# Optimization experiments

Hardware: AMD Instinct MI355X
Metric: run time of the kernel (lower is better)

## Reference

```python
import jax, jax.numpy as jnp
import numpy as np

B, S, D, H = 4, 1024, 1024, 16
DH = D // H
THETA = 10000.0
LAMBDA_INIT = 0.2  # layer 0: 0.8 - 0.6*exp(-0.3*0)
EPS = 1e-5


def setup_inputs() -> dict:
    key = jax.random.key(0)
    ks = jax.random.split(key, 10)
    s = 0.02
    return {
        "x_norm": jax.random.normal(ks[0], (B, S, D), jnp.float32),
        "affinity_a": jax.random.uniform(ks[1], (B, S - 1), jnp.float32, 0.5, 1.0),
        "Wq": jax.random.normal(ks[2], (2 * D, D), jnp.float32) * s,
        "bq": jnp.zeros((2 * D,), jnp.float32),
        "Wk": jax.random.normal(ks[3], (2 * D, D), jnp.float32) * s,
        "bk": jnp.zeros((2 * D,), jnp.float32),
        "Wv": jax.random.normal(ks[4], (D, D), jnp.float32) * s,
        "bv": jnp.zeros((D,), jnp.float32),
        "Wo": jax.random.normal(ks[5], (D, D), jnp.float32) * s,
        "bo": jnp.zeros((D,), jnp.float32),
        "gn_w": jnp.ones((D,), jnp.float32),
        "gn_b": jnp.zeros((D,), jnp.float32),
        "lam": jnp.float32(0.5),
    }


def _rope(x):
    # x: [B, H, S, DH]; rotate-half RoPE as in the torch module
    pos = jnp.arange(S, dtype=jnp.float32)
    freqs = 1.0 / (THETA ** (jnp.arange(0, DH, 2, dtype=jnp.float32) / DH))
    ang = pos[:, None] * freqs[None, :]          # [S, DH/2]
    cos, sin = jnp.cos(ang), jnp.sin(ang)
    x1, x2 = x[..., : DH // 2], x[..., DH // 2 :]
    return jnp.concatenate([x1 * cos - x2 * sin, x1 * sin + x2 * cos], axis=-1)


def _hier_mask(a):
    # C[b,i,j] = prod_{k=min(i,j)}^{max(i,j)-1} a[b,k]; diag = 1.
    # Vectorized via prefix log-sum instead of the O(S^2) python loop.
    logL = jnp.concatenate([jnp.zeros((a.shape[0], 1), a.dtype), jnp.cumsum(jnp.log(a), axis=1)], axis=1)  # [B, S]
    diff = logL[:, None, :] - logL[:, :, None]   # [B, i, j] = L_j - L_i
    upper = jnp.arange(S)[None, :] >= jnp.arange(S)[:, None]
    return jnp.exp(jnp.where(upper, diff, -diff))  # [B, S, S]


def _split_heads(t):
    return t.reshape(B, S, H, DH).transpose(0, 2, 1, 3)  # [B,H,S,DH]


def reference(x_norm, affinity_a, Wq, bq, Wk, bk, Wv, bv, Wo, bo, gn_w, gn_b, lam):
    qp = x_norm @ Wq.T + bq                      # [B,S,2D]
    kp = x_norm @ Wk.T + bk
    vp = x_norm @ Wv.T + bv                      # [B,S,D]
    q1, q2 = _split_heads(qp[..., :D]), _split_heads(qp[..., D:])
    k1, k2 = _split_heads(kp[..., :D]), _split_heads(kp[..., D:])
    v = _split_heads(vp)

    q1, k1, q2, k2 = _rope(q1), _rope(k1), _rope(q2), _rope(k2)

    scale = 1.0 / jnp.sqrt(jnp.float32(DH))
    a1 = jax.nn.softmax(jnp.einsum("bhid,bhjd->bhij", q1, k1) * scale, axis=-1)
    a2 = jax.nn.softmax(jnp.einsum("bhid,bhjd->bhij", q2, k2) * scale, axis=-1)

    C = _hier_mask(affinity_a)[:, None]          # [B,1,S,S]
    combined = C * (a1 - lam * a2)               # [B,H,S,S]
    ctx = jnp.einsum("bhij,bhjd->bhid", combined, v)   # [B,H,S,DH]
    ctx = ctx.transpose(0, 2, 1, 3).reshape(B, S, D)

    # GroupNorm(n_heads, d_model) applied over [B, D, S]: per (batch, group)
    # stats over the group's DH channels AND all S positions.
    xr = ctx.reshape(B, S, H, DH)
    mean = xr.mean(axis=(1, 3), keepdims=True)
    var = ((xr - mean) ** 2).mean(axis=(1, 3), keepdims=True)
    normed = (xr - mean) / jnp.sqrt(var + EPS)
    normed = normed * gn_w.reshape(1, 1, H, DH) + gn_b.reshape(1, 1, H, DH)
    normed = normed.reshape(B, S, D)

    scaled = normed * (1.0 - LAMBDA_INIT)
    return scaled @ Wo.T + bo                    # [B,S,D]
```

## Files before the change

### kernel.cpp

```cpp
#include <hip/hip_runtime.h>
#include <math.h>

typedef float  f32x4  __attribute__((ext_vector_type(4)));
typedef short  bf16x8 __attribute__((ext_vector_type(8)));
typedef unsigned short u16;

__device__ __forceinline__ u16 f2b(float f) {
  union { float f; unsigned u; } v; v.f = f;
  unsigned r = v.u + 0x7FFFu + ((v.u >> 16) & 1u);
  return (u16)(r >> 16);
}
__device__ __forceinline__ float b2f(u16 h) {
  union { unsigned u; float f; } v; v.u = ((unsigned)h) << 16;
  return v.f;
}

__device__ __forceinline__ void gl_lds16(const u16* g, u16* l) {
  __builtin_amdgcn_global_load_lds(
      (const __attribute__((address_space(1))) unsigned*)g,
      (__attribute__((address_space(3))) unsigned*)l, 16, 0, 0);
}

__global__ __launch_bounds__(256) void convert_kernel(
    const float* __restrict__ x,  const float* __restrict__ Wq,
    const float* __restrict__ Wk, const float* __restrict__ Wv,
    const float* __restrict__ Wo, const float* __restrict__ bq,
    const float* __restrict__ bk, const float* __restrict__ bv,
    const float* __restrict__ aff,
    u16* __restrict__ xb, u16* __restrict__ Wcat, u16* __restrict__ Wob,
    float* __restrict__ bcat, float* __restrict__ logL,
    float* __restrict__ ctab, float* __restrict__ stab)
{
  int bid = blockIdx.x;
  if (bid < 10245) {
    long i = ((long)bid * 256 + threadIdx.x) * 4;
    if (i < 10485760L) {
      const float* src; u16* dst; long o;
      if (i < 4194304L)      { src = x;  dst = xb;             o = i; }
      else if (i < 6291456L) { src = Wq; dst = Wcat;           o = i - 4194304L; }
      else if (i < 8388608L) { src = Wk; dst = Wcat + 2097152; o = i - 6291456L; }
      else if (i < 9437184L) { src = Wv; dst = Wcat + 4194304; o = i - 8388608L; }
      else                   { src = Wo; dst = Wob;            o = i - 9437184L; }
      float4 v = *(const float4*)(src + o);
      union { u16 h[4]; uint2 u2; } p;
      p.h[0] = f2b(v.x); p.h[1] = f2b(v.y); p.h[2] = f2b(v.z); p.h[3] = f2b(v.w);
      *(uint2*)(dst + o) = p.u2;
    } else if (i < 10490880L) {
      long j = i - 10485760L;
      const float* src; long o;
      if (j < 2048)      { src = bq; o = j; }
      else if (j < 4096) { src = bk; o = j - 2048; }
      else               { src = bv; o = j - 4096; }
      *(float4*)(bcat + j) = *(const float4*)(src + o);
    }
  } else if (bid < 10249) {
    __shared__ float sh[256];
    int b = bid - 10245, t = threadIdx.x;
    float c0, c1, c2, c3;
    {
      int i0 = 4 * t;
      float l0 = (i0 == 0) ? 0.f : log2f(aff[b * 1023 + i0 - 1]);
      float l1 = log2f(aff[b * 1023 + i0]);
      float l2 = log2f(aff[b * 1023 + i0 + 1]);
      float l3 = log2f(aff[b * 1023 + i0 + 2]);
      c0 = l0; c1 = c0 + l1; c2 = c1 + l2; c3 = c2 + l3;
    }
    sh[t] = c3;
    __syncthreads();
    for (int off = 1; off < 256; off <<= 1) {
      float add = (t >= off) ? sh[t - off] : 0.f;
      __syncthreads();
      sh[t] += add;
      __syncthreads();
    }
    float base = sh[t] - c3;
    float* Lp = logL + b * 1024 + 4 * t;
    Lp[0] = base + c0; Lp[1] = base + c1; Lp[2] = base + c2; Lp[3] = base + c3;
  } else {
    int idx = (bid - 10249) * 256 + threadIdx.x;
    int s = idx >> 5, i = idx & 31;
    float freq = expf(-(float)i * (9.210340371976184f / 32.f));
    float ang = (float)s * freq;
    ctab[idx] = cosf(ang);
    stab[idx] = sinf(ang);
  }
}

template<int EPI>
__global__ __launch_bounds__(256) void gemm_nt(
    const u16* __restrict__ A, const u16* __restrict__ Bw,
    const float* __restrict__ bias, float* __restrict__ outF,
    u16* __restrict__ q1t, u16* __restrict__ q2t,
    u16* __restrict__ k1t, u16* __restrict__ k2t, u16* __restrict__ vtT,
    const float* __restrict__ ctab, const float* __restrict__ stab,
    int N)
{
  const int K = 1024;
  __shared__ u16 As[128 * 64];
  __shared__ u16 Bs[128 * 64];
  int tid  = threadIdx.x;
  int lane = tid & 63, wave = tid >> 6;
  int wm = wave >> 1, wn = wave & 1;
  int m0 = blockIdx.y * 128, n0 = blockIdx.x * 128;
  int fr = lane & 15, hi = lane >> 4;

  int ac_r[4], ac_sb[4], cb_[4];
#pragma unroll
  for (int p = 0; p < 4; ++p) {
    int c = p * 256 + wave * 64 + lane;
    ac_r[p]  = c >> 3;
    ac_sb[p] = (c & 7) ^ (ac_r[p] & 7);
    cb_[p]   = (p * 256 + wave * 64) * 8;
  }

  f32x4 acc[4][4];
#pragma unroll
  for (int i = 0; i < 4; ++i)
#pragma unroll
    for (int j = 0; j < 4; ++j) acc[i][j] = 0.0f;

  for (int kk0 = 0; kk0 < K; kk0 += 64) {
    __syncthreads();
#pragma unroll
    for (int p = 0; p < 4; ++p) {
      gl_lds16(A  + (size_t)(m0 + ac_r[p]) * K + kk0 + ac_sb[p] * 8, &As[cb_[p]]);
      gl_lds16(Bw + (size_t)(n0 + ac_r[p]) * K + kk0 + ac_sb[p] * 8, &Bs[cb_[p]]);
    }
    __syncthreads();
#pragma unroll
    for (int ks = 0; ks < 2; ++ks) {
      bf16x8 af[4], bfv[4];
#pragma unroll
      for (int f = 0; f < 4; ++f) {
        int ra = wm * 64 + f * 16 + fr;
        int rb = wn * 64 + f * 16 + fr;
        int cba = (ks * 4 + hi) ^ (ra & 7);
        int cbb = (ks * 4 + hi) ^ (rb & 7);
        af[f]  = *(const bf16x8*)&As[ra * 64 + (cba << 3)];
        bfv[f] = *(const bf16x8*)&Bs[rb * 64 + (cbb << 3)];
      }
#pragma unroll
      for (int i = 0; i < 4; ++i)
#pragma unroll
        for (int j = 0; j < 4; ++j)
          acc[i][j] = __builtin_amdgcn_mfma_f32_16x16x32_bf16(af[i], bfv[j], acc[i][j], 0, 0, 0);
    }
  }

  int rg = lane >> 4;
  if (EPI == 0) {
    if (n0 < 4096) {
      u16* dst; int base;
      if (n0 < 1024)      { dst = q1t; base = 0; }
      else if (n0 < 2048) { dst = q2t; base = 1024; }
      else if (n0 < 3072) { dst = k1t; base = 2048; }
      else                { dst = k2t; base = 3072; }
      float qs = (n0 < 2048) ? 0.18033688011112042f : 1.0f;
#pragma unroll
      for (int i = 0; i < 4; ++i) {
#pragma unroll
        for (int e = 0; e < 4; ++e) {
          int m = m0 + wm * 64 + i * 16 + rg * 4 + e;
          int b = m >> 10, s = m & 1023;
#pragma unroll
          for (int j = 0; j < 2; ++j) {
            int n_lo = n0 + wn * 64 + j * 16 + fr;
            int feat = n_lo - base;
            int h = feat >> 6, dh = feat & 63;
            float a1 = acc[i][j][e]     + bias[n_lo];
            float a2 = acc[i][j + 2][e] + bias[n_lo + 32];
            float cs = ctab[s * 32 + dh], sn = stab[s * 32 + dh];
            float r0 = (a1 * cs - a2 * sn) * qs;
            float r1 = (a1 * sn + a2 * cs) * qs;
            unsigned pk;
            asm("v_cvt_pk_bf16_f32 %0, %1, %2" : "=v"(pk) : "v"(r0), "v"(r1));
            size_t rowb = ((size_t)(b * 16 + h) * 1024 + s) * 64;
            *(unsigned*)&dst[rowb + 2 * dh] = pk;
          }
        }
      }
    } else {
#pragma unroll
      for (int i = 0; i < 4; ++i) {
        int mbase = m0 + wm * 64 + i * 16 + rg * 4;
        int b = mbase >> 10, s0 = mbase & 1023;
#pragma unroll
        for (int j = 0; j < 4; ++j) {
          int n = n0 + wn * 64 + j * 16 + fr;
          int feat = n - 4096;
          int h = feat >> 6, dh = feat & 63;
          float bv = bias[n];
          union { u16 hh[4]; uint2 u2; } p;
#pragma unroll
          for (int e = 0; e < 4; ++e) p.hh[e] = f2b(acc[i][j][e] + bv);
          *(uint2*)&vtT[((size_t)(b * 16 + h) * 64 + dh) * 1024 + s0] = p.u2;
        }
      }
    }
  } else {
#pragma unroll
    for (int i = 0; i < 4; ++i)
#pragma unroll
      for (int j = 0; j < 4; ++j)
#pragma unroll
        for (int e = 0; e < 4; ++e) {
          int m = m0 + wm * 64 + i * 16 + rg * 4 + e;
          int n = n0 + wn * 64 + j * 16 + fr;
          outF[(size_t)m * N + n] = acc[i][j][e] + bias[n];
        }
  }
}

__global__ __launch_bounds__(256) void attn_fused(
    const u16* __restrict__ q1t, const u16* __restrict__ q2t,
    const u16* __restrict__ k1t, const u16* __restrict__ k2t,
    const u16* __restrict__ vtT,
    const float* __restrict__ logL, const float* __restrict__ lamp,
    u16* __restrict__ ctxb, float2* __restrict__ partials)
{
  __shared__ u16 K1s[64][72];
  __shared__ u16 K2s[64][72];
  __shared__ u16 Vts[64][72];
  __shared__ float lred1[2][2][32];
  __shared__ float lred2[2][2][32];
  __shared__ float pred[4][2];

  int tid  = threadIdx.x;
  int lane = tid & 63, wave = tid >> 6;
  int wm = wave >> 1, wn = wave & 1;
  int id = blockIdx.x;
  int bh = (id & 7) * 8 + (id >> 7);
  int q0 = ((id >> 3) & 15) * 64;
  int b = bh >> 4;
  int fr = lane & 15, hi = lane >> 4;

  bf16x8 qf1[2][2], qf2[2][2];
#pragma unroll
  for (int i = 0; i < 2; ++i)
#pragma unroll
    for (int ks = 0; ks < 2; ++ks) {
      size_t off = ((size_t)bh * 1024 + q0 + wm * 32 + i * 16 + fr) * 64 + ks * 32 + hi * 8;
      qf1[i][ks] = *(const bf16x8*)(q1t + off);
      qf2[i][ks] = *(const bf16x8*)(q2t + off);
    }
  float Lq[2][4];
#pragma unroll
  for (int i = 0; i < 2; ++i)
#pragma unroll
    for (int r = 0; r < 4; ++r)
      Lq[i][r] = logL[b * 1024 + q0 + wm * 32 + i * 16 + hi * 4 + r];

  float Lq_top = logL[b * 1024 + q0];
  float Lq_bot = logL[b * 1024 + q0 + 63];

  float lacc1[2][4], lacc2[2][4];
  f32x4 U1[2][2], U2[2][2];
#pragma unroll
  for (int i = 0; i < 2; ++i)
#pragma unroll
    for (int r = 0; r < 4; ++r) { lacc1[i][r] = 0.f; lacc2[i][r] = 0.f; }
#pragma unroll
  for (int i = 0; i < 2; ++i)
#pragma unroll
    for (int j = 0; j < 2; ++j) { U1[i][j] = 0.f; U2[i][j] = 0.f; }

  int sr = tid >> 2, sc0 = (tid & 3) * 16;
  int swz = (sr >> 3) & 7;
  int blk0 = ((sc0 >> 3) ^ swz) << 3;
  int blk1 = (((sc0 >> 3) + 1) ^ swz) << 3;

  unsigned a1base = (unsigned)(size_t)&K1s[wm * 32 + hi * 4][wn * 32 + fr];
  unsigned a2base = (unsigned)(size_t)&K2s[wm * 32 + hi * 4][wn * 32 + fr];

  for (int kt = 0; kt < 16; ++kt) {
    int ktop = kt * 64;
    float maxc;
    if (ktop > q0 + 63)      maxc = logL[b * 1024 + ktop] - Lq_bot;
    else if (ktop + 63 < q0) maxc = Lq_top - logL[b * 1024 + ktop + 63];
    else                     maxc = 0.f;
    bool far = (maxc < -24.f);

    __syncthreads();
    size_t gb = ((size_t)bh * 1024 + kt * 64 + sr) * 64 + sc0;
    bf16x8 a0 = *(const bf16x8*)(k1t + gb), a1 = *(const bf16x8*)(k1t + gb + 8);
    bf16x8 b0 = *(const bf16x8*)(k2t + gb), b1 = *(const bf16x8*)(k2t + gb + 8);
    *(bf16x8*)&K1s[sr][sc0] = a0;  *(bf16x8*)&K1s[sr][sc0 + 8] = a1;
    *(bf16x8*)&K2s[sr][sc0] = b0;  *(bf16x8*)&K2s[sr][sc0 + 8] = b1;
    if (!far) {
      size_t gv = (size_t)bh * 65536 + (size_t)sr * 1024 + kt * 64 + sc0;
      bf16x8 v0 = *(const bf16x8*)(vtT + gv), v1 = *(const bf16x8*)(vtT + gv + 8);
      *(bf16x8*)&Vts[sr][blk0] = v0;  *(bf16x8*)&Vts[sr][blk1] = v1;
    }
    __syncthreads();

    f32x4 S1[2][2], S2[2][2];
#pragma unroll
    for (int i = 0; i < 2; ++i)
#pragma unroll
      for (int j = 0; j < 2; ++j) { S1[i][j] = 0.f; S2[i][j] = 0.f; }
    __builtin_amdgcn_s_setprio(1);
#pragma unroll
    for (int ks = 0; ks < 2; ++ks) {
      bf16x8 kf1[2], kf2[2];
#pragma unroll
      for (int j = 0; j < 2; ++j) {
        kf1[j] = *(const bf16x8*)&K1s[wn * 32 + j * 16 + fr][ks * 32 + hi * 8];
        kf2[j] = *(const bf16x8*)&K2s[wn * 32 + j * 16 + fr][ks * 32 + hi * 8];
      }
#pragma unroll
      for (int i = 0; i < 2; ++i)
#pragma unroll
        for (int j = 0; j < 2; ++j) {
          S1[i][j] = __builtin_amdgcn_mfma_f32_16x16x32_bf16(qf1[i][ks], kf1[j], S1[i][j], 0, 0, 0);
          S2[i][j] = __builtin_amdgcn_mfma_f32_16x16x32_bf16(qf2[i][ks], kf2[j], S2[i][j], 0, 0, 0);
        }
    }
    __builtin_amdgcn_s_setprio(0);

    if (!far) {
      float Ltl[2];
#pragma unroll
      for (int j = 0; j < 2; ++j) Ltl[j] = logL[b * 1024 + kt * 64 + wn * 32 + j * 16 + fr];
      __syncthreads();

#pragma unroll
      for (int i = 0; i < 2; ++i) {
#pragma unroll
        for (int r = 0; r < 4; ++r) {
          float lq = Lq[i][r];
          float e1j[2], e2j[2], p1j[2], p2j[2];
#pragma unroll
          for (int j = 0; j < 2; ++j) {
            float nd = -fabsf(Ltl[j] - lq);
            float t1, t2, ec;
            asm("v_exp_f32 %0, %1" : "=v"(t1) : "v"(S1[i][j][r]));
            asm("v_exp_f32 %0, %1" : "=v"(t2) : "v"(S2[i][j][r]));
            asm("v_exp_f32 %0, %1" : "=v"(ec) : "v"(nd));
            e1j[j] = t1; e2j[j] = t2;
            p1j[j] = t1 * ec; p2j[j] = t2 * ec;
          }
          lacc1[i][r] += e1j[0] + e1j[1];
          lacc2[i][r] += e2j[0] + e2j[1];
          unsigned off = (unsigned)((i * 16 + r) * 144);
          unsigned ad1 = a1base + off, ad2 = a2base + off;
          unsigned pk1, pk2;
          asm("v_cvt_pk_bf16_f32 %0, %1, %2" : "=v"(pk1) : "v"(p1j[0]), "v"(p1j[1]));
          asm("v_cvt_pk_bf16_f32 %0, %1, %2" : "=v"(pk2) : "v"(p2j[0]), "v"(p2j[1]));
          asm volatile("ds_write_b16 %0, %1\n\tds_write_b16_d16_hi %0, %1 offset:32"
                       :: "v"(ad1), "v"(pk1) : "memory");
          asm volatile("ds_write_b16 %0, %1\n\tds_write_b16_d16_hi %0, %1 offset:32"
                       :: "v"(ad2), "v"(pk2) : "memory");
        }
      }
      __syncthreads();

      __builtin_amdgcn_s_setprio(1);
#pragma unroll
      for (int ks = 0; ks < 2; ++ks) {
        bf16x8 pa1[2], pa2[2], vb[2];
#pragma unroll
        for (int i = 0; i < 2; ++i) {
          pa1[i] = *(const bf16x8*)&K1s[wm * 32 + i * 16 + fr][ks * 32 + hi * 8];
          pa2[i] = *(const bf16x8*)&K2s[wm * 32 + i * 16 + fr][ks * 32 + hi * 8];
        }
#pragma unroll
        for (int j = 0; j < 2; ++j) {
          int row = wn * 32 + j * 16 + fr;
          int kbb = (ks * 4 + hi) ^ ((row >> 3) & 7);
          vb[j] = *(const bf16x8*)&Vts[row][kbb << 3];
        }
#pragma unroll
        for (int i = 0; i < 2; ++i)
#pragma unroll
          for (int j = 0; j < 2; ++j) {
            U1[i][j] = __builtin_amdgcn_mfma_f32_16x16x32_bf16(pa1[i], vb[j], U1[i][j], 0, 0, 0);
            U2[i][j] = __builtin_amdgcn_mfma_f32_16x16x32_bf16(pa2[i], vb[j], U2[i][j], 0, 0, 0);
          }
      }
      __builtin_amdgcn_s_setprio(0);
    } else {
#pragma unroll
      for (int i = 0; i < 2; ++i) {
#pragma unroll
        for (int r = 0; r < 4; ++r) {
          float t1a, t1b, t2a, t2b;
          asm("v_exp_f32 %0, %1" : "=v"(t1a) : "v"(S1[i][0][r]));
          asm("v_exp_f32 %0, %1" : "=v"(t1b) : "v"(S1[i][1][r]));
          asm("v_exp_f32 %0, %1" : "=v"(t2a) : "v"(S2[i][0][r]));
          asm("v_exp_f32 %0, %1" : "=v"(t2b) : "v"(S2[i][1][r]));
          lacc1[i][r] += t1a + t1b;
          lacc2[i][r] += t2a + t2b;
        }
      }
    }
  }

#pragma unroll
  for (int i = 0; i < 2; ++i)
#pragma unroll
    for (int r = 0; r < 4; ++r) {
#pragma unroll
      for (int m = 1; m < 16; m <<= 1) {
        lacc1[i][r] += __shfl_xor(lacc1[i][r], m);
        lacc2[i][r] += __shfl_xor(lacc2[i][r], m);
      }
    }
  if (fr == 0) {
#pragma unroll
    for (int i = 0; i < 2; ++i)
#pragma unroll
      for (int r = 0; r < 4; ++r) {
        int rl = i * 16 + hi * 4 + r;
        lred1[wn][wm][rl] = lacc1[i][r];
        lred2[wn][wm][rl] = lacc2[i][r];
      }
  }
  __syncthreads();
  float lam = lamp[0];

  float psum = 0.f, psq = 0.f;
#pragma unroll
  for (int i = 0; i < 2; ++i) {
#pragma unroll
    for (int r = 0; r < 4; ++r) {
      int rl = i * 16 + hi * 4 + r;
      float l1 = lred1[0][wm][rl] + lred1[1][wm][rl];
      float l2 = lred2[0][wm][rl] + lred2[1][wm][rl];
      float inv1 = 1.f / l1;
      float inv2 = lam / l2;
      int qg = q0 + wm * 32 + i * 16 + hi * 4 + r;
#pragma unroll
      for (int j = 0; j < 2; ++j) {
        int dh = wn * 32 + j * 16 + fr;
        float o = U1[i][j][r] * inv1 - U2[i][j][r] * inv2;
        ctxb[((size_t)bh * 1024 + qg) * 64 + dh] = f2b(o);
        psum += o; psq += o * o;
      }
    }
  }
#pragma unroll
  for (int m = 1; m < 64; m <<= 1) {
    psum += __shfl_xor(psum, m);
    psq  += __shfl_xor(psq, m);
  }
  if (lane == 0) { pred[wave][0] = psum; pred[wave][1] = psq; }
  __syncthreads();
  if (tid == 0)
    partials[id] = make_float2(pred[0][0] + pred[1][0] + pred[2][0] + pred[3][0],
                               pred[0][1] + pred[1][1] + pred[2][1] + pred[3][1]);
}

__global__ __launch_bounds__(256) void gn_apply(
    const u16* __restrict__ ctxb, const float2* __restrict__ partials,
    const float* __restrict__ gw, const float* __restrict__ gb,
    u16* __restrict__ normed)
{
  int tid = threadIdx.x;
  int srow = blockIdx.x;
  int b = srow >> 10;
  int h = tid >> 4, qi = tid & 15;
  int bh = b * 16 + h;
  float2 pp = partials[(bh & 7) * 128 + qi * 8 + (bh >> 3)];
  float s = pp.x, ss = pp.y;
#pragma unroll
  for (int o = 1; o < 16; o <<= 1) { s += __shfl_xor(s, o); ss += __shfl_xor(ss, o); }
  float mean = s * (1.f / 65536.f);
  float vinv = rsqrtf(ss * (1.f / 65536.f) - mean * mean + 1e-5f);

  unsigned d  = (unsigned)tid * 4u;
  unsigned dh = d & 63u;
  uint2 raw = *(const uint2*)&ctxb[(((size_t)bh) * 1024 + (srow & 1023)) * 64 + dh];
  const u16* rp = (const u16*)&raw;
  float4 g  = *(const float4*)&gw[d];
  float4 be = *(const float4*)&gb[d];
  union { u16 hh[4]; uint2 u2; } p;
  p.hh[0] = f2b(((b2f(rp[0]) - mean) * vinv * g.x + be.x) * 0.8f);
  p.hh[1] = f2b(((b2f(rp[1]) - mean) * vinv * g.y + be.y) * 0.8f);
  p.hh[2] = f2b(((b2f(rp[2]) - mean) * vinv * g.z + be.z) * 0.8f);
  p.hh[3] = f2b(((b2f(rp[3]) - mean) * vinv * g.w + be.w) * 0.8f);
  *(uint2*)&normed[(size_t)srow * 1024 + d] = p.u2;
}

extern "C" void kernel_launch(void* const* d_in, const int* in_sizes, int n_in,
                              void* d_out, int out_size, void* d_ws, size_t ws_size,
                              hipStream_t stream) {
  (void)in_sizes; (void)n_in; (void)out_size; (void)ws_size;
  const float* x   = (const float*)d_in[0];
  const float* aff = (const float*)d_in[1];
  const float* Wq  = (const float*)d_in[2];
  const float* bq  = (const float*)d_in[3];
  const float* Wk  = (const float*)d_in[4];
  const float* bk  = (const float*)d_in[5];
  const float* Wv  = (const float*)d_in[6];
  const float* bv  = (const float*)d_in[7];
  const float* Wo  = (const float*)d_in[8];
  const float* bo  = (const float*)d_in[9];
  const float* gw  = (const float*)d_in[10];
  const float* gb  = (const float*)d_in[11];
  const float* lam = (const float*)d_in[12];
  float* out = (float*)d_out;

  char* w = (char*)d_ws;
  u16*    xb    = (u16*)(w);
  u16*    Wcat  = (u16*)(w + 8388608);
  u16*    Wob   = (u16*)(w + 18874368);
  float*  bcat  = (float*)(w + 20971520);
  u16*    q1t   = (u16*)(w + 20992000);
  u16*    q2t   = (u16*)(w + 29380608);
  u16*    k1t   = (u16*)(w + 37769216);
  u16*    k2t   = (u16*)(w + 46157824);
  u16*    vtT   = (u16*)(w + 54546432);
  float*  logL  = (float*)(w + 62935040);
  float*  ctab  = (float*)(w + 62951424);
  float*  stab  = (float*)(w + 63082496);
  float2* parts = (float2*)(w + 63213568);
  u16*    ctxb  = (u16*)(w + 63475712);
  u16*    normed= (u16*)(w + 80253440);

  convert_kernel<<<10377, 256, 0, stream>>>(x, Wq, Wk, Wv, Wo, bq, bk, bv, aff,
                                            xb, Wcat, Wob, bcat, logL, ctab, stab);
  gemm_nt<0><<<dim3(40, 32), 256, 0, stream>>>(xb, Wcat, bcat, nullptr, q1t, q2t, k1t, k2t, vtT, ctab, stab, 5120);
  attn_fused<<<1024, 256, 0, stream>>>(q1t, q2t, k1t, k2t, vtT, logL, lam, ctxb, parts);
  gn_apply<<<4096, 256, 0, stream>>>(ctxb, parts, gw, gb, normed);
  gemm_nt<1><<<dim3(8, 32), 256, 0, stream>>>(normed, Wob, bo, out, nullptr, nullptr, nullptr, nullptr, nullptr, ctab, stab, 1024);
}
```

Baseline: 159.9 us.

## Fuse GroupNorm apply into output projection GEMM A-tile load

Removes the standalone gn_apply kernel and the normed intermediate buffer. The output GEMM now reads the bf16 context directly in head-major layout and applies a per-column affine transform (GroupNorm stats, gain, bias, 0.8 scale) while staging the A tile into LDS. This saves one launch and a write plus read of an 8MB tensor. In exchange, the A-operand loads become synchronous register loads with ALU work inside the K loop instead of async global-to-LDS copies, and the normalization is recomputed by each of the 8 N-blocks.

New measurement: 159.0 us, median of 2. About the same (-0.6%).

```diff
diff --git a/kernel.cpp b/kernel.cpp
--- a/kernel.cpp
+++ b/kernel.cpp
@@ -211,6 +211,125 @@
   }
 }
 
+__global__ __launch_bounds__(256) void gemm_out(
+    const u16* __restrict__ ctxb, const u16* __restrict__ Bw,
+    const float2* __restrict__ partials,
+    const float* __restrict__ gw, const float* __restrict__ gb,
+    const float* __restrict__ bias, float* __restrict__ outF)
+{
+  const int K = 1024, N = 1024;
+  __shared__ u16 As[128 * 64];
+  __shared__ u16 Bs[128 * 64];
+  __shared__ float acol[1024];
+  __shared__ float bcol[1024];
+  __shared__ float2 mvs[16];
+
+  int tid  = threadIdx.x;
+  int lane = tid & 63, wave = tid >> 6;
+  int wm = wave >> 1, wn = wave & 1;
+  int m0 = blockIdx.y * 128, n0 = blockIdx.x * 128;
+  int fr = lane & 15, hi = lane >> 4;
+  int b = m0 >> 10;
+
+  {
+    int h = tid >> 4, qi = tid & 15;
+    int bh = b * 16 + h;
+    float2 pp = partials[(bh & 7) * 128 + qi * 8 + (bh >> 3)];
+    float s = pp.x, ss = pp.y;
+#pragma unroll
+    for (int o = 1; o < 16; o <<= 1) { s += __shfl_xor(s, o); ss += __shfl_xor(ss, o); }
+    if (qi == 0) {
+      float mean = s * (1.f / 65536.f);
+      float vinv = rsqrtf(ss * (1.f / 65536.f) - mean * mean + 1e-5f);
+      mvs[h] = make_float2(mean, vinv);
+    }
+  }
+  __syncthreads();
+  {
+    int col = tid * 4;
+    float4 g  = *(const float4*)&gw[col];
+    float4 be = *(const float4*)&gb[col];
+    float2 mv = mvs[col >> 6];
+    float a0 = mv.y * g.x * 0.8f, a1 = mv.y * g.y * 0.8f;
+    float a2 = mv.y * g.z * 0.8f, a3 = mv.y * g.w * 0.8f;
+    acol[col+0] = a0; bcol[col+0] = 0.8f * be.x - mv.x * a0;
+    acol[col+1] = a1; bcol[col+1] = 0.8f * be.y - mv.x * a1;
+    acol[col+2] = a2; bcol[col+2] = 0.8f * be.z - mv.x * a2;
+    acol[col+3] = a3; bcol[col+3] = 0.8f * be.w - mv.x * a3;
+  }
+
+  int ac_r[4], ac_sb[4], cb_[4];
+#pragma unroll
+  for (int p = 0; p < 4; ++p) {
+    int c = p * 256 + wave * 64 + lane;
+    ac_r[p]  = c >> 3;
+    ac_sb[p] = (c & 7) ^ (ac_r[p] & 7);
+    cb_[p]   = (p * 256 + wave * 64) * 8;
+  }
+
+  f32x4 acc[4][4];
+#pragma unroll
+  for (int i = 0; i < 4; ++i)
+#pragma unroll
+    for (int j = 0; j < 4; ++j) acc[i][j] = 0.0f;
+
+  for (int kk0 = 0; kk0 < K; kk0 += 64) {
+    __syncthreads();
+#pragma unroll
+    for (int p = 0; p < 4; ++p) {
+      gl_lds16(Bw + (size_t)(n0 + ac_r[p]) * K + kk0 + ac_sb[p] * 8, &Bs[cb_[p]]);
+      int row = m0 + ac_r[p];
+      int s   = row & 1023;
+      int c0  = kk0 + ac_sb[p] * 8;
+      int h   = kk0 >> 6;
+      uint4 raw = *(const uint4*)&ctxb[(((size_t)(b * 16 + h)) * 1024 + s) * 64 + (c0 & 63)];
+      const u16* rp = (const u16*)&raw;
+      float av[8];
+#pragma unroll
+      for (int e = 0; e < 8; ++e)
+        av[e] = b2f(rp[e]) * acol[c0 + e] + bcol[c0 + e];
+      unsigned pk0, pk1, pk2, pk3;
+      asm("v_cvt_pk_bf16_f32 %0, %1, %2" : "=v"(pk0) : "v"(av[0]), "v"(av[1]));
+      asm("v_cvt_pk_bf16_f32 %0, %1, %2" : "=v"(pk1) : "v"(av[2]), "v"(av[3]));
+      asm("v_cvt_pk_bf16_f32 %0, %1, %2" : "=v"(pk2) : "v"(av[4]), "v"(av[5]));
+      asm("v_cvt_pk_bf16_f32 %0, %1, %2" : "=v"(pk3) : "v"(av[6]), "v"(av[7]));
+      uint4 w4; w4.x = pk0; w4.y = pk1; w4.z = pk2; w4.w = pk3;
+      *(uint4*)&As[cb_[p] + lane * 8] = w4;
+    }
+    __syncthreads();
+#pragma unroll
+    for (int ks = 0; ks < 2; ++ks) {
+      bf16x8 af[4], bfv[4];
+#pragma unroll
+      for (int f = 0; f < 4; ++f) {
+        int ra = wm * 64 + f * 16 + fr;
+        int rb = wn * 64 + f * 16 + fr;
+        int cba = (ks * 4 + hi) ^ (ra & 7);
+        int cbb = (ks * 4 + hi) ^ (rb & 7);
+        af[f]  = *(const bf16x8*)&As[ra * 64 + (cba << 3)];
+        bfv[f] = *(const bf16x8*)&Bs[rb * 64 + (cbb << 3)];
+      }
+#pragma unroll
+      for (int i = 0; i < 4; ++i)
+#pragma unroll
+        for (int j = 0; j < 4; ++j)
+          acc[i][j] = __builtin_amdgcn_mfma_f32_16x16x32_bf16(af[i], bfv[j], acc[i][j], 0, 0, 0);
+    }
+  }
+
+  int rg = lane >> 4;
+#pragma unroll
+  for (int i = 0; i < 4; ++i)
+#pragma unroll
+    for (int j = 0; j < 4; ++j)
+#pragma unroll
+      for (int e = 0; e < 4; ++e) {
+        int m = m0 + wm * 64 + i * 16 + rg * 4 + e;
+        int n = n0 + wn * 64 + j * 16 + fr;
+        outF[(size_t)m * N + n] = acc[i][j][e] + bias[n];
+      }
+}
+
 __global__ __launch_bounds__(256) void attn_fused(
     const u16* __restrict__ q1t, const u16* __restrict__ q2t,
     const u16* __restrict__ k1t, const u16* __restrict__ k2t,
@@ -450,37 +569,6 @@
                                pred[0][1] + pred[1][1] + pred[2][1] + pred[3][1]);
 }
 
-__global__ __launch_bounds__(256) void gn_apply(
-    const u16* __restrict__ ctxb, const float2* __restrict__ partials,
-    const float* __restrict__ gw, const float* __restrict__ gb,
-    u16* __restrict__ normed)
-{
-  int tid = threadIdx.x;
-  int srow = blockIdx.x;
-  int b = srow >> 10;
-  int h = tid >> 4, qi = tid & 15;
-  int bh = b * 16 + h;
-  float2 pp = partials[(bh & 7) * 128 + qi * 8 + (bh >> 3)];
-  float s = pp.x, ss = pp.y;
-#pragma unroll
-  for (int o = 1; o < 16; o <<= 1) { s += __shfl_xor(s, o); ss += __shfl_xor(ss, o); }
-  float mean = s * (1.f / 65536.f);
-  float vinv = rsqrtf(ss * (1.f / 65536.f) - mean * mean + 1e-5f);
-
-  unsigned d  = (unsigned)tid * 4u;
-  unsigned dh = d & 63u;
-  uint2 raw = *(const uint2*)&ctxb[(((size_t)bh) * 1024 + (srow & 1023)) * 64 + dh];
-  const u16* rp = (const u16*)&raw;
-  float4 g  = *(const float4*)&gw[d];
-  float4 be = *(const float4*)&gb[d];
-  union { u16 hh[4]; uint2 u2; } p;
-  p.hh[0] = f2b(((b2f(rp[0]) - mean) * vinv * g.x + be.x) * 0.8f);
-  p.hh[1] = f2b(((b2f(rp[1]) - mean) * vinv * g.y + be.y) * 0.8f);
-  p.hh[2] = f2b(((b2f(rp[2]) - mean) * vinv * g.z + be.z) * 0.8f);
-  p.hh[3] = f2b(((b2f(rp[3]) - mean) * vinv * g.w + be.w) * 0.8f);
-  *(uint2*)&normed[(size_t)srow * 1024 + d] = p.u2;
-}
-
 extern "C" void kernel_launch(void* const* d_in, const int* in_sizes, int n_in,
                               void* d_out, int out_size, void* d_ws, size_t ws_size,
                               hipStream_t stream) {
@@ -515,12 +603,10 @@
   float*  stab  = (float*)(w + 63082496);
   float2* parts = (float2*)(w + 63213568);
   u16*    ctxb  = (u16*)(w + 63475712);
-  u16*    normed= (u16*)(w + 80253440);
 
   convert_kernel<<<10377, 256, 0, stream>>>(x, Wq, Wk, Wv, Wo, bq, bk, bv, aff,
                                             xb, Wcat, Wob, bcat, logL, ctab, stab);
   gemm_nt<0><<<dim3(40, 32), 256, 0, stream>>>(xb, Wcat, bcat, nullptr, q1t, q2t, k1t, k2t, vtT, ctab, stab, 5120);
   attn_fused<<<1024, 256, 0, stream>>>(q1t, q2t, k1t, k2t, vtT, logL, lam, ctxb, parts);
-  gn_apply<<<4096, 256, 0, stream>>>(ctxb, parts, gw, gb, normed);
-  gemm_nt<1><<<dim3(8, 32), 256, 0, stream>>>(normed, Wob, bo, out, nullptr, nullptr, nullptr, nullptr, nullptr, ctab, stab, 1024);
-}
+  gemm_out<<<dim3(8, 32), 256, 0, stream>>>(ctxb, Wob, parts, gw, gb, bo, out);
+}
```
